# Optimization experiments

Hardware: AMD Instinct MI355X
Metric: run time of the kernel (lower is better)

The kernel has to match this reference:

```python
import jax, jax.numpy as jnp
import numpy as np

N = 50000          # num nodes
E = 800000         # num edges (avg degree 16)
C_IN = 64          # input channels
TOWERS = 4
F_IN = C_IN // TOWERS       # 16 (divide_input=True)
OUT = 128
F_OUT = OUT // TOWERS       # 32
NUM_AGG = 4                 # mean, std, max, min
NUM_SC = 3                  # identity, amplification, attenuation
AVG_LOG_DEG = float(np.log(17.0))  # deg histogram: all nodes degree 16 -> log(16+1)


def setup_inputs() -> dict:
    key = jax.random.key(0)
    ks = jax.random.split(key, 10)
    nodes = jax.random.normal(ks[0], (N, C_IN), dtype=jnp.float32)
    senders = jax.random.randint(ks[1], (E,), 0, N)
    receivers = jax.random.randint(ks[2], (E,), 0, N)
    # per-tower pre-MLP: Linear(2*F_IN -> F_IN), pre_layers=1 (no activation)
    pre_w = jax.random.normal(ks[3], (TOWERS, 2 * F_IN, F_IN), dtype=jnp.float32) / np.sqrt(2 * F_IN)
    pre_b = jnp.zeros((TOWERS, F_IN), dtype=jnp.float32)
    # per-tower post-MLP: Linear(F_IN + F_IN*12 -> F_OUT), post_layers=1
    post_in = F_IN + F_IN * NUM_AGG * NUM_SC  # 208
    post_w = jax.random.normal(ks[4], (TOWERS, post_in, F_OUT), dtype=jnp.float32) / np.sqrt(post_in)
    post_b = jnp.zeros((TOWERS, F_OUT), dtype=jnp.float32)
    # final linear: TOWERS*F_OUT -> OUT
    lin_w = jax.random.normal(ks[5], (TOWERS * F_OUT, OUT), dtype=jnp.float32) / np.sqrt(TOWERS * F_OUT)
    lin_b = jnp.zeros((OUT,), dtype=jnp.float32)
    return {"nodes": nodes, "senders": senders, "receivers": receivers,
            "pre_w": pre_w, "pre_b": pre_b, "post_w": post_w, "post_b": post_b,
            "lin_w": lin_w, "lin_b": lin_b}


def reference(nodes, senders, receivers, pre_w, pre_b, post_w, post_b, lin_w, lin_b):
    # divide_input=True: split channels across towers -> [N, T, F_IN]
    x = nodes.reshape(N, TOWERS, F_IN)
    x_i = x[senders]                                  # [E, T, F_IN]
    x_j = x[receivers]                                # [E, T, F_IN]
    h = jnp.concatenate([x_i, x_j], axis=-1)          # [E, T, 2*F_IN]
    # per-tower pre-MLP (single linear), vectorized over towers
    msg = jnp.einsum('etf,tfo->eto', h, pre_w) + pre_b  # [E, T, F_IN]

    # degree-scaled multi-aggregator segment reduce over receivers
    count = jax.ops.segment_sum(jnp.ones((E,), dtype=msg.dtype), receivers, num_segments=N)  # [N]
    d = jnp.clip(count, 1.0, None)
    inv_d = (1.0 / d)[:, None, None]
    mean = jax.ops.segment_sum(msg, receivers, num_segments=N) * inv_d           # [N,T,F]
    mean_sq = jax.ops.segment_sum(msg * msg, receivers, num_segments=N) * inv_d
    std = jnp.sqrt(jax.nn.relu(mean_sq - mean * mean) + 1e-5)
    has_nb = (count > 0)[:, None, None]
    mx = jax.ops.segment_max(msg, receivers, num_segments=N)
    mx = jnp.where(has_nb, mx, 0.0)
    mn = -jax.ops.segment_max(-msg, receivers, num_segments=N)
    mn = jnp.where(has_nb, mn, 0.0)
    agg = jnp.concatenate([mean, std, mx, mn], axis=-1)  # [N, T, 4*F_IN]

    # scalers: identity, amplification, attenuation (degree clamped to >= 1)
    log_d = jnp.log(d + 1.0)[:, None, None]
    amp = log_d / AVG_LOG_DEG
    att = AVG_LOG_DEG / log_d
    scaled = jnp.concatenate([agg, agg * amp, agg * att], axis=-1)  # [N, T, 12*F_IN]

    out = jnp.concatenate([x, scaled], axis=-1)                     # [N, T, 13*F_IN]
    outs = jnp.einsum('ntf,tfo->nto', out, post_w) + post_b         # [N, T, F_OUT]
    flat = outs.reshape(N, TOWERS * F_OUT)                          # [N, 128]
    return flat @ lin_w + lin_b                                     # [N, OUT]
```

## Files before the change

### kernel.cpp

```cpp
#include <hip/hip_runtime.h>

#define AVG_LOG_DEG 2.8332133440562162f
#define CAP 64
#define CSTRIDE 16

typedef __attribute__((ext_vector_type(8))) short short8;
typedef __attribute__((ext_vector_type(4))) float f32x4;

static __device__ __forceinline__ float bl(unsigned u) { return __uint_as_float(u << 16); }
static __device__ __forceinline__ float bh(unsigned u) { return __uint_as_float(u & 0xffff0000u); }
static __device__ __forceinline__ unsigned short f2b(float f) {
    unsigned u = __float_as_uint(f);
    return (unsigned short)((u + 0x7fffu + ((u >> 16) & 1u)) >> 16);
}
static __device__ __forceinline__ unsigned pk(unsigned short lo, unsigned short hi) {
    return (unsigned)lo | ((unsigned)hi << 16);
}


__global__ __launch_bounds__(256) void k_setup(
    const float* __restrict__ nodes, const float* __restrict__ pre_w,
    const float* __restrict__ pre_b,
    const float* __restrict__ post_w, const float* __restrict__ lin_w,
    unsigned short* __restrict__ Yh, float* __restrict__ H,
    unsigned short* __restrict__ postT,
    unsigned short* __restrict__ linT, int* __restrict__ cursor,
    int n, int A, int n16)
{
    int b = blockIdx.x;
    if (b < A) {
        int lane = threadIdx.x & 63;
        int node = b * 4 + (threadIdx.x >> 6);
        if (node >= n) return;
        int t = lane >> 4, f = lane & 15;
        float w0[16], w1[16];
        #pragma unroll
        for (int k = 0; k < 16; ++k) {
            w0[k] = pre_w[(t * 32 + k) * 16 + f];
            w1[k] = pre_w[(t * 32 + 16 + k) * 16 + f];
        }
        const float4* xp = reinterpret_cast<const float4*>(nodes + (size_t)node * 64 + t * 16);
        float4 x0 = xp[0], x1 = xp[1], x2 = xp[2], x3 = xp[3];
        float xs[16] = {x0.x, x0.y, x0.z, x0.w, x1.x, x1.y, x1.z, x1.w,
                        x2.x, x2.y, x2.z, x2.w, x3.x, x3.y, x3.z, x3.w};
        float y = 0.f;
        float h = pre_b[t * 16 + f];
        #pragma unroll
        for (int k = 0; k < 16; ++k) {
            y = fmaf(xs[k], w0[k], y);
            h = fmaf(xs[k], w1[k], h);
        }
        Yh[(size_t)node * 64 + lane] = f2b(y);
        H[(size_t)node * 64 + lane] = h;
    } else if (b < A + 176) {
        int i = (b - A) * 256 + threadIdx.x;
        if (i < 28672) {
            int t = i / (32 * 224);
            int r = i % (32 * 224);
            int nn = r / 224;
            int k = r % 224;
            float wv;
            if (k < 192)      wv = post_w[((size_t)t * 208 + 16 + k) * 32 + nn];
            else if (k < 208) wv = post_w[((size_t)t * 208 + (k - 192)) * 32 + nn];
            else              wv = 0.f;
            postT[i] = f2b(wv);
        }
        int j = i - 28672;
        if (j >= 0 && j < 16384) {
            int nn = j >> 7, k = j & 127;
            linT[j] = f2b(lin_w[k * 128 + nn]);
        }
    } else {
        int i = (b - A - 176) * 1024 + threadIdx.x * 4;
        if (i < n16) {
            int4 z; z.x = z.y = z.z = z.w = 0;
            *reinterpret_cast<int4*>(cursor + i) = z;
        }
    }
}


__global__ __launch_bounds__(256) void k_scatter2(
    const int* __restrict__ send, const int* __restrict__ recv,
    int* __restrict__ cursor, int* __restrict__ slots,
    int e)
{
    int i0 = (blockIdx.x * 256 + threadIdx.x) * 2;
    int2 rv, sv;
    if (i0 + 1 < e) {
        rv = *reinterpret_cast<const int2*>(recv + i0);
        sv = *reinterpret_cast<const int2*>(send + i0);
    } else {
        rv.x = rv.y = -1; sv.x = sv.y = 0;
        if (i0 < e) { rv.x = recv[i0]; sv.x = send[i0]; }
    }
    int p0 = 0, p1 = 0;
    if (rv.x >= 0) p0 = atomicAdd(&cursor[(size_t)rv.x * CSTRIDE], 1);
    if (rv.y >= 0) p1 = atomicAdd(&cursor[(size_t)rv.y * CSTRIDE], 1);
    if (rv.x >= 0 && p0 < CAP) slots[(size_t)rv.x * CAP + p0] = sv.x;
    if (rv.y >= 0 && p1 < CAP) slots[(size_t)rv.y * CAP + p1] = sv.y;
}


__global__ __launch_bounds__(256) void k_agg(
    const int* __restrict__ cursor,
    const int* __restrict__ slots,
    const unsigned short* __restrict__ Yh,
    const float* __restrict__ H,
    unsigned short* __restrict__ aggh, int n)
{
    int lane = threadIdx.x & 63;
    int node = blockIdx.x * 4 + (threadIdx.x >> 6);
    if (node >= n) return;
    int t = lane >> 4, f = lane & 15;

    int idxv = slots[(size_t)node * CAP + lane];
    float hjw = H[(size_t)node * 64 + lane];
    int d = min(cursor[(size_t)node * CSTRIDE], CAP);
    const unsigned short* Yl = Yh + lane;

    float s = 0.f, s2 = 0.f, mx = -INFINITY, mn = INFINITY;
    int e = 0;
    for (; e + 16 <= d; e += 16) {
        unsigned v[16];
        #pragma unroll
        for (int q = 0; q < 16; ++q) {
            int si = __builtin_amdgcn_readlane(idxv, e + q);
            v[q] = Yl[(size_t)si * 64];
        }
        #pragma unroll
        for (int q = 0; q < 16; ++q) {
            float m = __uint_as_float(v[q] << 16) + hjw;
            s += m;
            s2 = fmaf(m, m, s2);
            mx = fmaxf(mx, m);
            mn = fminf(mn, m);
        }
    }
    int rem = d - e;
    if (rem > 0) {
        unsigned v[16];
        #pragma unroll
        for (int q = 0; q < 16; ++q) {
            int si = __builtin_amdgcn_readlane(idxv, min(e + q, d - 1));
            v[q] = Yl[(size_t)si * 64];
        }
        #pragma unroll
        for (int q = 0; q < 16; ++q) {
            if (q < rem) {
                float m = __uint_as_float(v[q] << 16) + hjw;
                s += m;
                s2 = fmaf(m, m, s2);
                mx = fmaxf(mx, m);
                mn = fminf(mn, m);
            }
        }
    }

    float dc = fmaxf((float)d, 1.f);
    float inv = 1.f / dc;
    float mean = s * inv;
    float var = fmaf(-mean, mean, s2 * inv);
    float sd = sqrtf(fmaxf(var, 0.f) + 1e-5f);
    if (d == 0) { mx = 0.f; mn = 0.f; }

    unsigned short* ag = aggh + (size_t)node * 256 + t * 64 + f;
    ag[0]  = f2b(mean);
    ag[16] = f2b(sd);
    ag[32] = f2b(mx);
    ag[48] = f2b(mn);
}


__global__ __launch_bounds__(256, 3) void k_post(
    const float* __restrict__ nodes,
    const unsigned short* __restrict__ aggh,
    const int* __restrict__ deg,
    const unsigned short* __restrict__ postT,
    const unsigned short* __restrict__ linT,
    const float* __restrict__ post_b,
    const float* __restrict__ lin_b,
    float* __restrict__ out, int n)
{
    __shared__ unsigned short sV[32 * 256];
    __shared__ unsigned short sFlat[32 * 128];
    __shared__ float sAmp[32], sAtt[32];

    int tid = threadIdx.x;
    int n0 = blockIdx.x * 32;

    if (tid < 32) {
        int g = min(n0 + tid, n - 1);
        float dc = fmaxf((float)min(deg[(size_t)g * CSTRIDE], CAP), 1.f);
        float ld = logf(dc + 1.f);
        sAmp[tid] = ld * (1.f / AVG_LOG_DEG);
        sAtt[tid] = AVG_LOG_DEG / ld;
    }

    int w = tid >> 6, lane = tid & 63;
    int quad = lane >> 4, mr = lane & 15;
    int mstrip = w & 1, nhalf = w >> 1;
    int nn = tid >> 3, j8 = tid & 7;
    int sw = nn & 7;
    int gn = min(n0 + nn, n - 1);
    int rsw = mr & 7;

    uint4 pa4[4];
    #pragma unroll
    for (int t = 0; t < 4; ++t)
        pa4[t] = *reinterpret_cast<const uint4*>(aggh + (size_t)gn * 256 + t * 64 + j8 * 8);

    uint4 xw4[4];
    #pragma unroll
    for (int t = 0; t < 4; ++t) { xw4[t].x = 0; xw4[t].y = 0; xw4[t].z = 0; xw4[t].w = 0; }
    if (j8 < 2) {
        #pragma unroll
        for (int t = 0; t < 4; ++t) {
            const float4* xp = reinterpret_cast<const float4*>(nodes + (size_t)gn * 64 + t * 16 + j8 * 8);
            float4 xa = xp[0], xb = xp[1];
            xw4[t].x = pk(f2b(xa.x), f2b(xa.y)); xw4[t].y = pk(f2b(xa.z), f2b(xa.w));
            xw4[t].z = pk(f2b(xb.x), f2b(xb.y)); xw4[t].w = pk(f2b(xb.z), f2b(xb.w));
        }
    }

    const unsigned short* bbase = postT + (size_t)(nhalf * 16 + mr) * 224 + quad * 8;
    short8 bA[7], bB[7];
    #pragma unroll
    for (int kk = 0; kk < 7; ++kk) bA[kk] = *reinterpret_cast<const short8*>(bbase + kk * 32);
    #pragma unroll
    for (int kk = 0; kk < 7; ++kk) bB[kk] = *reinterpret_cast<const short8*>(bbase + 32 * 224 + kk * 32);

    __syncthreads();
    float ampv = sAmp[nn], attv = sAtt[nn];

    #pragma unroll
    for (int t = 0; t < 4; ++t) {
        {
            unsigned short* row = &sV[nn * 256];
            uint4 a = pa4[t];
            *reinterpret_cast<uint4*>(row + (j8 ^ sw) * 8) = a;
            unsigned uu[4] = {a.x, a.y, a.z, a.w};
            unsigned short pa[8], pb[8];
            #pragma unroll
            for (int q = 0; q < 4; ++q) {
                float lo = bl(uu[q]), hi = bh(uu[q]);
                pa[2*q]   = f2b(lo * ampv); pa[2*q+1] = f2b(hi * ampv);
                pb[2*q]   = f2b(lo * attv); pb[2*q+1] = f2b(hi * attv);
            }
            uint4 wa, wb;
            wa.x = pk(pa[0], pa[1]); wa.y = pk(pa[2], pa[3]);
            wa.z = pk(pa[4], pa[5]); wa.w = pk(pa[6], pa[7]);
            wb.x = pk(pb[0], pb[1]); wb.y = pk(pb[2], pb[3]);
            wb.z = pk(pb[4], pb[5]); wb.w = pk(pb[6], pb[7]);
            *reinterpret_cast<uint4*>(row + (8  + (j8 ^ sw)) * 8) = wa;
            *reinterpret_cast<uint4*>(row + (16 + (j8 ^ sw)) * 8) = wb;
            *reinterpret_cast<uint4*>(row + (24 + (j8 ^ sw)) * 8) = xw4[t];
        }
        __syncthreads();

        f32x4 acc = {0.f, 0.f, 0.f, 0.f};
        const unsigned short* av0 = &sV[(mstrip * 16 + mr) * 256];
        #pragma unroll
        for (int kk = 0; kk < 7; ++kk) {
            int c = kk * 4 + quad;
            int pc = (c & ~7) | ((c & 7) ^ rsw);
            short8 avv = *reinterpret_cast<const short8*>(av0 + pc * 8);
            if (t & 1) acc = __builtin_amdgcn_mfma_f32_16x16x32_bf16(avv, bB[kk], acc, 0, 0, 0);
            else       acc = __builtin_amdgcn_mfma_f32_16x16x32_bf16(avv, bA[kk], acc, 0, 0, 0);
        }

        if (t == 0) {
            #pragma unroll
            for (int kk = 0; kk < 7; ++kk)
                bA[kk] = *reinterpret_cast<const short8*>(bbase + 2 * 32 * 224 + kk * 32);
        } else if (t == 1) {
            #pragma unroll
            for (int kk = 0; kk < 7; ++kk)
                bB[kk] = *reinterpret_cast<const short8*>(bbase + 3 * 32 * 224 + kk * 32);
        }

        int col = t * 32 + nhalf * 16 + mr;
        float pbv = post_b[col];
        int cc = col >> 3, co = col & 7;
        #pragma unroll
        for (int i = 0; i < 4; ++i) {
            int rowf = mstrip * 16 + quad * 4 + i;
            int pc = (cc & ~7) | ((cc & 7) ^ (rowf & 7));
            sFlat[rowf * 128 + pc * 8 + co] = f2b(acc[i] + pbv);
        }
        __syncthreads();
    }

    f32x4 facc[4];
    #pragma unroll
    for (int nt = 0; nt < 4; ++nt) { facc[nt].x = 0.f; facc[nt].y = 0.f; facc[nt].z = 0.f; facc[nt].w = 0.f; }

    const unsigned short* af0 = &sFlat[(mstrip * 16 + mr) * 128];
    #pragma unroll
    for (int kk = 0; kk < 4; ++kk) {
        int c = kk * 4 + quad;
        int pc = (c & ~7) | ((c & 7) ^ rsw);
        short8 avv = *reinterpret_cast<const short8*>(af0 + pc * 8);
        #pragma unroll
        for (int nt = 0; nt < 4; ++nt) {
            short8 bv = *reinterpret_cast<const short8*>(
                linT + (size_t)(nhalf * 64 + nt * 16 + mr) * 128 + kk * 32 + quad * 8);
            facc[nt] = __builtin_amdgcn_mfma_f32_16x16x32_bf16(avv, bv, facc[nt], 0, 0, 0);
        }
    }

    #pragma unroll
    for (int nt = 0; nt < 4; ++nt) {
        int col = nhalf * 64 + nt * 16 + mr;
        float lb = lin_b[col];
        #pragma unroll
        for (int i = 0; i < 4; ++i) {
            int node = n0 + mstrip * 16 + quad * 4 + i;
            if (node < n) out[(size_t)node * 128 + col] = facc[nt][i] + lb;
        }
    }
}

extern "C" void kernel_launch(void* const* d_in, const int* in_sizes, int n_in,
                              void* d_out, int out_size, void* d_ws, size_t ws_size,
                              hipStream_t stream)
{
    const float* nodes  = (const float*)d_in[0];
    const int*   send   = (const int*)d_in[1];
    const int*   recv   = (const int*)d_in[2];
    const float* pre_w  = (const float*)d_in[3];
    const float* pre_b  = (const float*)d_in[4];
    const float* post_w = (const float*)d_in[5];
    const float* post_b = (const float*)d_in[6];
    const float* lin_w  = (const float*)d_in[7];
    const float* lin_b  = (const float*)d_in[8];
    float* out = (float*)d_out;

    int N = in_sizes[0] / 64;
    int E = in_sizes[1];
    int Npad = (N + 255) & ~255;

    int* cursor = (int*)d_ws;
    int* slots  = cursor + (size_t)Npad * CSTRIDE;
    unsigned short* Yh = (unsigned short*)(slots + (size_t)Npad * CAP);
    float* H = (float*)(Yh + (size_t)Npad * 64);
    unsigned short* aggh  = (unsigned short*)(H + (size_t)Npad * 64);
    unsigned short* postT = aggh + (size_t)Npad * 256;
    unsigned short* linT  = postT + 28672;

    int n16 = Npad * CSTRIDE;
    int nbZ = (n16 + 1023) / 1024;
    int A = (N + 3) / 4;
    int nbS = (E / 2 + 255) / 256 + 1;

    k_setup   <<<A + 176 + nbZ, 256, 0, stream>>>(nodes, pre_w, pre_b, post_w, lin_w,
                                                  Yh, H, postT, linT, cursor, N, A, n16);
    k_scatter2<<<nbS, 256, 0, stream>>>(send, recv, cursor, slots, E);
    k_agg     <<<(N + 3) / 4, 256, 0, stream>>>(cursor, slots, Yh, H, aggh, N);
    k_post    <<<(N + 31) / 32, 256, 0, stream>>>(nodes, aggh, cursor, postT, linT,
                                                  post_b, lin_b, out, N);
}
```

Measured before the change: 215.8 us.

## Pre-bin edges by receiver mod 8 before atomic slot scatter

Adds a k_bin pass that partitions edges into 8 buckets by receiver low bits, using wave ballots and a shared-memory stage so the bucketed array is written in coalesced runs. k_scatter2 then walks each bucket from a fixed set of blocks, so the atomics and slot writes from one block hit a subset of nodes. This is meant to improve locality and reduce contention on the cursor atomics. It costs an extra kernel launch plus a full read and write of the edge list. k_setup's node projection also now has each wave loop over 16 nodes, reusing the pre_w registers instead of reloading them per node.

```diff
diff --git a/kernel.cpp b/kernel.cpp
--- a/kernel.cpp
+++ b/kernel.cpp
@@ -25,13 +25,12 @@
     unsigned short* __restrict__ Yh, float* __restrict__ H,
     unsigned short* __restrict__ postT,
     unsigned short* __restrict__ linT, int* __restrict__ cursor,
-    int n, int A, int n16)
+    int n, int A, int nZ)
 {
     int b = blockIdx.x;
     if (b < A) {
         int lane = threadIdx.x & 63;
-        int node = b * 4 + (threadIdx.x >> 6);
-        if (node >= n) return;
+        int wid = threadIdx.x >> 6;
         int t = lane >> 4, f = lane & 15;
         float w0[16], w1[16];
         #pragma unroll
@@ -39,19 +38,25 @@
             w0[k] = pre_w[(t * 32 + k) * 16 + f];
             w1[k] = pre_w[(t * 32 + 16 + k) * 16 + f];
         }
-        const float4* xp = reinterpret_cast<const float4*>(nodes + (size_t)node * 64 + t * 16);
-        float4 x0 = xp[0], x1 = xp[1], x2 = xp[2], x3 = xp[3];
-        float xs[16] = {x0.x, x0.y, x0.z, x0.w, x1.x, x1.y, x1.z, x1.w,
-                        x2.x, x2.y, x2.z, x2.w, x3.x, x3.y, x3.z, x3.w};
-        float y = 0.f;
-        float h = pre_b[t * 16 + f];
-        #pragma unroll
-        for (int k = 0; k < 16; ++k) {
-            y = fmaf(xs[k], w0[k], y);
-            h = fmaf(xs[k], w1[k], h);
-        }
-        Yh[(size_t)node * 64 + lane] = f2b(y);
-        H[(size_t)node * 64 + lane] = h;
+        float hb = pre_b[t * 16 + f];
+        int nbase = b * 64 + wid * 16;
+        for (int jj = 0; jj < 16; ++jj) {
+            int node = nbase + jj;
+            if (node >= n) break;
+            const float4* xp = reinterpret_cast<const float4*>(nodes + (size_t)node * 64 + t * 16);
+            float4 x0 = xp[0], x1 = xp[1], x2 = xp[2], x3 = xp[3];
+            float xs[16] = {x0.x, x0.y, x0.z, x0.w, x1.x, x1.y, x1.z, x1.w,
+                            x2.x, x2.y, x2.z, x2.w, x3.x, x3.y, x3.z, x3.w};
+            float y = 0.f;
+            float h = hb;
+            #pragma unroll
+            for (int k = 0; k < 16; ++k) {
+                y = fmaf(xs[k], w0[k], y);
+                h = fmaf(xs[k], w1[k], h);
+            }
+            Yh[(size_t)node * 64 + lane] = f2b(y);
+            H[(size_t)node * 64 + lane] = h;
+        }
     } else if (b < A + 176) {
         int i = (b - A) * 256 + threadIdx.x;
         if (i < 28672) {
@@ -72,7 +77,7 @@
         }
     } else {
         int i = (b - A - 176) * 1024 + threadIdx.x * 4;
-        if (i < n16) {
+        if (i < nZ) {
             int4 z; z.x = z.y = z.z = z.w = 0;
             *reinterpret_cast<int4*>(cursor + i) = z;
         }
@@ -80,25 +85,106 @@
 }
 
 
+__global__ __launch_bounds__(256) void k_bin(
+    const int* __restrict__ send, const int* __restrict__ recv,
+    int* __restrict__ bktCnt, int2* __restrict__ bktArr,
+    int e, int eCap)
+{
+    __shared__ int2 stage[2048];
+    __shared__ int wcnt[4][8], wbase[4][8], btot[8], bbase[8], pref[9];
+
+    int tid = threadIdx.x;
+    int lane = tid & 63, wid = tid >> 6;
+    int base = blockIdx.x * 2048 + wid * 512 + lane;
+
+    int rv[8], sv[8], rk[8];
+    unsigned long long lt = (1ULL << lane) - 1ULL;
+    unsigned long long runLo = 0, runHi = 0;
+
+    #pragma unroll
+    for (int q = 0; q < 8; ++q) {
+        int idx = base + q * 64;
+        bool valid = idx < e;
+        rv[q] = valid ? recv[idx] : 0;
+        sv[q] = valid ? send[idx] : 0;
+        int bb = rv[q] & 7;
+        unsigned long long m0 = __ballot(bb & 1);
+        unsigned long long m1 = __ballot(bb & 2);
+        unsigned long long m2 = __ballot(bb & 4);
+        unsigned long long mv = __ballot(valid);
+        unsigned long long mo = ((bb & 1) ? m0 : ~m0) & ((bb & 2) ? m1 : ~m1)
+                              & ((bb & 4) ? m2 : ~m2) & mv;
+        unsigned long long sel = (bb & 4) ? runHi : runLo;
+        int runb = (int)((sel >> ((bb & 3) * 16)) & 0xffffULL);
+        rk[q] = runb + __popcll(mo & lt);
+        unsigned long long addLo = 0, addHi = 0;
+        #pragma unroll
+        for (int k = 0; k < 4; ++k) {
+            unsigned long long mkl = ((k & 1) ? m0 : ~m0) & ((k & 2) ? m1 : ~m1) & ~m2 & mv;
+            unsigned long long mkh = ((k & 1) ? m0 : ~m0) & ((k & 2) ? m1 : ~m1) &  m2 & mv;
+            addLo |= (unsigned long long)__popcll(mkl) << (k * 16);
+            addHi |= (unsigned long long)__popcll(mkh) << (k * 16);
+        }
+        runLo += addLo; runHi += addHi;
+        if (!valid) rk[q] = -1;
+    }
+    if (lane < 8) {
+        unsigned long long sel = (lane & 4) ? runHi : runLo;
+        wcnt[wid][lane] = (int)((sel >> ((lane & 3) * 16)) & 0xffffULL);
+    }
+    __syncthreads();
+    if (tid < 8) {
+        int c0 = wcnt[0][tid], c1 = wcnt[1][tid], c2 = wcnt[2][tid], c3 = wcnt[3][tid];
+        wbase[0][tid] = 0;
+        wbase[1][tid] = c0;
+        wbase[2][tid] = c0 + c1;
+        wbase[3][tid] = c0 + c1 + c2;
+        int bt = c0 + c1 + c2 + c3;
+        btot[tid] = bt;
+        bbase[tid] = atomicAdd(&bktCnt[tid], bt);
+    }
+    __syncthreads();
+    if (tid == 0) {
+        int acc = 0;
+        #pragma unroll
+        for (int k = 0; k < 8; ++k) { pref[k] = acc; acc += btot[k]; }
+        pref[8] = acc;
+    }
+    __syncthreads();
+    #pragma unroll
+    for (int q = 0; q < 8; ++q) {
+        if (rk[q] >= 0) {
+            int bb = rv[q] & 7;
+            int pos = pref[bb] + wbase[wid][bb] + rk[q];
+            int2 ed; ed.x = rv[q]; ed.y = sv[q];
+            stage[pos] = ed;
+        }
+    }
+    __syncthreads();
+    int tot = pref[8];
+    for (int i = tid; i < tot; i += 256) {
+        int k = 0;
+        #pragma unroll
+        for (int j = 1; j < 8; ++j) k += (i >= pref[j]);
+        int g = bbase[k] + (i - pref[k]);
+        if (g < eCap)
+            bktArr[(size_t)k * eCap + g] = stage[i];
+    }
+}
+
+
 __global__ __launch_bounds__(256) void k_scatter2(
-    const int* __restrict__ send, const int* __restrict__ recv,
-    int* __restrict__ cursor, int* __restrict__ slots,
-    int e)
-{
-    int i0 = (blockIdx.x * 256 + threadIdx.x) * 2;
-    int2 rv, sv;
-    if (i0 + 1 < e) {
-        rv = *reinterpret_cast<const int2*>(recv + i0);
-        sv = *reinterpret_cast<const int2*>(send + i0);
-    } else {
-        rv.x = rv.y = -1; sv.x = sv.y = 0;
-        if (i0 < e) { rv.x = recv[i0]; sv.x = send[i0]; }
-    }
-    int p0 = 0, p1 = 0;
-    if (rv.x >= 0) p0 = atomicAdd(&cursor[(size_t)rv.x * CSTRIDE], 1);
-    if (rv.y >= 0) p1 = atomicAdd(&cursor[(size_t)rv.y * CSTRIDE], 1);
-    if (rv.x >= 0 && p0 < CAP) slots[(size_t)rv.x * CAP + p0] = sv.x;
-    if (rv.y >= 0 && p1 < CAP) slots[(size_t)rv.y * CAP + p1] = sv.y;
+    const int* __restrict__ bktCnt, const int2* __restrict__ bktArr,
+    int* __restrict__ cursor, int* __restrict__ slots, int eCap)
+{
+    int bkt = blockIdx.x & 7;
+    int cnt = min(bktCnt[bkt], eCap);
+    const int2* ba = bktArr + (size_t)bkt * eCap;
+    for (int i = (blockIdx.x >> 3) * 256 + threadIdx.x; i < cnt; i += 256 * 256) {
+        int2 ed = ba[i];
+        int p = atomicAdd(&cursor[(size_t)ed.x * CSTRIDE], 1);
+        if (p < CAP) slots[(size_t)ed.x * CAP + p] = ed.y;
+    }
 }
 
 
@@ -341,21 +427,24 @@
     int Npad = (N + 255) & ~255;
 
     int* cursor = (int*)d_ws;
-    int* slots  = cursor + (size_t)Npad * CSTRIDE;
+    int* bktCnt = cursor + (size_t)Npad * CSTRIDE;
+    int2* bktArr = (int2*)(bktCnt + 256);
+    int* slots  = (int*)(bktArr + (size_t)8 * E);
     unsigned short* Yh = (unsigned short*)(slots + (size_t)Npad * CAP);
     float* H = (float*)(Yh + (size_t)Npad * 64);
     unsigned short* aggh  = (unsigned short*)(H + (size_t)Npad * 64);
     unsigned short* postT = aggh + (size_t)Npad * 256;
     unsigned short* linT  = postT + 28672;
 
-    int n16 = Npad * CSTRIDE;
-    int nbZ = (n16 + 1023) / 1024;
-    int A = (N + 3) / 4;
-    int nbS = (E / 2 + 255) / 256 + 1;
+    int nZ = Npad * CSTRIDE + 256;
+    int nbZ = (nZ + 1023) / 1024;
+    int A = (N + 63) / 64;
+    int nbBin = (E + 2047) / 2048;
 
     k_setup   <<<A + 176 + nbZ, 256, 0, stream>>>(nodes, pre_w, pre_b, post_w, lin_w,
-                                                  Yh, H, postT, linT, cursor, N, A, n16);
-    k_scatter2<<<nbS, 256, 0, stream>>>(send, recv, cursor, slots, E);
+                                                  Yh, H, postT, linT, cursor, N, A, nZ);
+    k_bin     <<<nbBin, 256, 0, stream>>>(send, recv, bktCnt, bktArr, E, E);
+    k_scatter2<<<2048, 256, 0, stream>>>(bktCnt, bktArr, cursor, slots, E);
     k_agg     <<<(N + 3) / 4, 256, 0, stream>>>(cursor, slots, Yh, H, aggh, N);
     k_post    <<<(N + 31) / 32, 256, 0, stream>>>(nodes, aggh, cursor, postT, linT,
                                                   post_b, lin_b, out, N);
```

Result: faster. 205.0 us (-5.0%).
